# Kernel tuning notes

Measured on AMD Instinct MI355X. Metric: run time of the kernel, lower is better.

## Reference

```python
import jax, jax.numpy as jnp
import numpy as np
from jax import lax


def _kaiming_uniform(key, shape):
    fan_in = shape[1]
    bound = np.sqrt(6.0 / fan_in)
    return jax.random.uniform(key, shape, jnp.float32, -bound, bound)


def rbf_conv(x, w, k, pad):
    # x: [B,C,H,W]; w: [O, C*k*k]. Equivalent to F.unfold + torch.cdist (p=2).
    patches = lax.conv_general_dilated_patches(
        x, (k, k), (1, 1), [(pad, pad), (pad, pad)])  # [B, C*k*k, Ho, Wo]
    B, D, Ho, Wo = patches.shape
    p = patches.reshape(B, D, Ho * Wo)                 # [B, D, L]
    pn = jnp.sum(p * p, axis=1)                        # [B, L]
    wn = jnp.sum(w * w, axis=1)                        # [O]
    cross = jnp.einsum('bdl,od->bol', p, w)            # [B, O, L]
    d2 = pn[:, None, :] + wn[None, :, None] - 2.0 * cross
    d = jnp.sqrt(jnp.maximum(d2, 0.0))
    return d.reshape(B, w.shape[0], Ho, Wo)


def sfm(x, alpha):
    # non-overlapping (fh,fw) blocks, elementwise alpha weight, mean-pool
    B, C, H, W = x.shape
    fh, fw = alpha.shape
    xb = x.reshape(B, C, H // fh, fh, W // fw, fw).transpose(0, 1, 2, 4, 3, 5)
    return jnp.mean(xb * alpha, axis=(-2, -1))         # [B,C,H//fh,W//fw]


def gauss_act(d, std):
    return jnp.exp(d * d / (-2.0 * std * std))


def crelu(x, bias):
    return x * (x >= bias).astype(x.dtype)


def basic_block(x, w, std, bias, alpha, k, pad):
    d = rbf_conv(x, w, k, pad)
    return sfm(crelu(gauss_act(d, std), bias), alpha)


def setup_inputs() -> dict:
    key = jax.random.key(0)
    ks = jax.random.split(key, 8)
    x = jax.random.normal(ks[0], (16, 3, 128, 128), jnp.float32)
    w1 = _kaiming_uniform(ks[1], (96, 3 * 5 * 5))
    w2 = _kaiming_uniform(ks[2], (192, 96 * 5 * 5))
    w3 = _kaiming_uniform(ks[3], (384, 192 * 3 * 3))
    alpha = jnp.linspace(0.9, 0.99, 4, dtype=jnp.float32).reshape(2, 2)
    fc_w = jax.random.normal(ks[4], (100, 384 * 32 * 32), jnp.float32) * 0.01
    fc_b = jnp.zeros((100,), jnp.float32)
    return {
        'x': x,
        'w1': w1, 'std1': jnp.array([2.0], jnp.float32), 'bias1': jnp.array([0.3], jnp.float32), 'alpha1': alpha,
        'w2': w2, 'std2': jnp.array([2.0], jnp.float32), 'bias2': jnp.array([0.3], jnp.float32), 'alpha2': alpha,
        'w3': w3, 'std3': jnp.array([2.0], jnp.float32), 'bias3': jnp.array([0.3], jnp.float32),
        'fc_w': fc_w, 'fc_b': fc_b,
    }


def reference(x, w1, std1, bias1, alpha1, w2, std2, bias2, alpha2,
              w3, std3, bias3, fc_w, fc_b):
    h = basic_block(x, w1, std1, bias1, alpha1, 5, 2)      # [16,96,64,64]
    h = basic_block(h, w2, std2, bias2, alpha2, 5, 2)      # [16,192,32,32]
    d = rbf_conv(h, w3, 3, 1)                              # [16,384,32,32]
    h = crelu(gauss_act(d, std3), bias3)
    out = h.reshape(x.shape[0], -1) @ fc_w.T + fc_b        # [16,100]
    return out
```

## Files before the change

### kernel.cpp

```cpp
#include <hip/hip_runtime.h>

#define TPB 256

typedef short bf16x8 __attribute__((ext_vector_type(8)));
typedef float f32x4 __attribute__((ext_vector_type(4)));

__device__ inline unsigned short f2bf(float f) {
    unsigned int u = __float_as_uint(f);
    unsigned int r = (u + 0x7fffu + ((u >> 16) & 1u)) >> 16;
    return (unsigned short)r;
}
__device__ inline float bf2f(unsigned short h) {
    return __uint_as_float(((unsigned int)h) << 16);
}

__device__ __forceinline__ void gl16(void* lds, const void* g) {
    __builtin_amdgcn_global_load_lds(
        (const __attribute__((address_space(1))) unsigned int*)g,
        (__attribute__((address_space(3))) unsigned int*)lds, 16, 0, 0);
}

__global__ void prep_all(const float* __restrict__ x,
                         const float* __restrict__ w1, const float* __restrict__ w2,
                         const float* __restrict__ w3,
                         unsigned short* __restrict__ xbf,
                         unsigned short* __restrict__ w1r, unsigned short* __restrict__ w2r,
                         unsigned short* __restrict__ w3r, unsigned short* __restrict__ zerob,
                         float* __restrict__ wn1, float* __restrict__ wn2,
                         float* __restrict__ wn3) {
    int bid = blockIdx.x;
    int tid = threadIdx.x;
    if (bid < 1024) {
        int idx = bid * TPB + tid;
        int b = idx >> 14, px = idx & 16383;
        const float* xb = x + (size_t)b * 3 * 16384 + px;
        float v0 = xb[0], v1 = xb[16384], v2 = xb[32768];
        ushort4 v;
        v.x = f2bf(v0); v.y = f2bf(v1); v.z = f2bf(v2);
        v.w = f2bf(v0 * v0 + v1 * v1 + v2 * v2);
        *(ushort4*)&xbf[(size_t)idx * 4] = v;
    } else if (bid < 4388) {
        int idx = (bid - 1024) * TPB + tid;
        if (idx < 13056) {
            int o = idx / 136, d = idx - o * 136;
            int tp = d >> 2, c = d & 3;
            float v = 0.f;
            if (tp < 30) {
                int ki = tp / 6, kj = tp - 6 * ki;
                if (kj < 5) v = (c < 3) ? w1[o * 75 + c * 25 + ki * 5 + kj] : -0.5f;
            }
            w1r[idx] = f2bf(v);
        } else if (idx < 492288) {
            int i = idx - 13056;
            int c = i & 31; int r = i >> 5;
            int o = r % 192; r /= 192;
            int tap = r % 26; int cg = r / 26;
            float v = 0.f;
            if (tap < 25) v = w2[((size_t)o * 96 + cg * 32 + c) * 25 + tap];
            w2r[i] = f2bf(v);
        } else if (idx < 860928) {
            int i = idx - 492288;
            int c = i & 31; int r = i >> 5;
            int o = r % 192; r /= 192;
            int tap = r % 10; int cg = r / 10;
            float v = 0.f;
            if (tap < 9) v = w3[((size_t)o * 192 + cg * 32 + c) * 9 + tap];
            w3r[i] = f2bf(v);
        } else if (idx < 860992) {
            zerob[idx - 860928] = 0;
        }
    } else {
        int o = (bid - 4388) * 4 + (tid >> 6);
        int lane = tid & 63;
        const float* row; float* dst; int D;
        if (o < 96)       { row = w1 + (size_t)o * 75;           D = 75;   dst = wn1 + o; }
        else if (o < 288) { int r = o - 96;  row = w2 + (size_t)r * 2400; D = 2400; dst = wn2 + r; }
        else              { int r = o - 288; row = w3 + (size_t)r * 1728; D = 1728; dst = wn3 + r; }
        float acc = 0.f;
        for (int i = lane; i < D; i += 64) { float v = row[i]; acc += v * v; }
        #pragma unroll
        for (int off = 32; off >= 1; off >>= 1) acc += __shfl_down(acc, off);
        if (lane == 0) *dst = acc;
    }
}

__launch_bounds__(256, 2)
__global__ void conv1_mfma(const unsigned short* __restrict__ xbf,
                           const unsigned short* __restrict__ w1r,
                           const float* __restrict__ wn,
                           const float* __restrict__ stdp, const float* __restrict__ biasp,
                           const float* __restrict__ alphap,
                           unsigned short* __restrict__ out,
                           float* __restrict__ sqout)
{
    __shared__ unsigned short in_s[22 * 20 * 4];
    __shared__ unsigned short w_s[96 * 136];

    int bid = blockIdx.x;
    int tx = bid & 7; bid >>= 3;
    int ty = bid & 7; bid >>= 3;
    int b = bid;
    int x0 = tx * 16, y0 = ty * 16;
    int tid = threadIdx.x;
    int lane = tid & 63, wv = tid >> 6;
    int col = lane & 15, kg = lane >> 4;

    for (int idx = tid; idx < 21 * 20; idx += 256) {
        int py = idx / 20, px = idx - py * 20;
        int gy = y0 - 2 + py, gx = x0 - 2 + px;
        ushort4 v = make_ushort4(0, 0, 0, 0);
        if (gy >= 0 && gy < 128 && gx >= 0 && gx < 128)
            v = *(const ushort4*)&xbf[(((size_t)b * 128 + gy) * 128 + gx) * 4];
        *(ushort4*)&in_s[idx * 4] = v;
    }
    for (int idx = tid; idx < 1632; idx += 256)
        *(bf16x8*)&w_s[idx * 8] = *(const bf16x8*)&w1r[idx * 8];
    __syncthreads();

    f32x4 acc[6][4];
    #pragma unroll
    for (int mt = 0; mt < 6; ++mt)
        #pragma unroll
        for (int n = 0; n < 4; ++n) acc[mt][n] = (f32x4){0.f, 0.f, 0.f, 0.f};

    #pragma unroll
    for (int ks = 0; ks < 4; ++ks) {
        int tap0 = ks * 8 + kg * 2;
        int ki = tap0 / 6, kj = tap0 - 6 * ki;
        bf16x8 bfrag[4];
        #pragma unroll
        for (int n = 0; n < 4; ++n) {
            int row = wv * 4 + n + ki;
            int ix = col + kj;
            const unsigned short* p = &in_s[(row * 20 + ix) * 4];
            union { bf16x8 v; uint2 u[2]; } tmp;
            tmp.u[0] = *(const uint2*)p;
            tmp.u[1] = *(const uint2*)(p + 4);
            bfrag[n] = tmp.v;
        }
        bf16x8 afrag[6];
        #pragma unroll
        for (int mt = 0; mt < 6; ++mt)
            afrag[mt] = *(const bf16x8*)&w_s[(mt * 16 + col) * 136 + ks * 32 + kg * 8];
        #pragma unroll
        for (int mt = 0; mt < 6; ++mt)
            #pragma unroll
            for (int n = 0; n < 4; ++n)
                acc[mt][n] = __builtin_amdgcn_mfma_f32_16x16x32_bf16(
                    afrag[mt], bfrag[n], acc[mt][n], 0, 0, 0);
    }

    float stdv = stdp[0], biasv = biasp[0];
    float inv2s2 = 1.f / (2.f * stdv * stdv);
    float a00 = alphap[0], a01 = alphap[1], a10 = alphap[2], a11 = alphap[3];
    int dx = col & 1;
    float ax0 = dx ? a01 : a00;
    float ax1 = dx ? a11 : a10;

    float sqa[2] = {0.f, 0.f};
    #pragma unroll
    for (int mt = 0; mt < 6; ++mt) {
        #pragma unroll
        for (int p2 = 0; p2 < 2; ++p2) {
            unsigned short res[4];
            #pragma unroll
            for (int r = 0; r < 4; ++r) {
                int o = mt * 16 + kg * 4 + r;
                float wno = wn[o];
                float d20 = fmaxf(wno - 2.f * acc[mt][2 * p2][r], 0.f);
                float d21 = fmaxf(wno - 2.f * acc[mt][2 * p2 + 1][r], 0.f);
                float g0 = __expf(-d20 * inv2s2);
                float g1 = __expf(-d21 * inv2s2);
                g0 = (g0 >= biasv) ? g0 : 0.f;
                g1 = (g1 >= biasv) ? g1 : 0.f;
                float s = ax0 * g0 + ax1 * g1;
                s += __shfl_xor(s, 1);
                res[r] = f2bf(0.25f * s);
                float vv = bf2f(res[r]);
                sqa[p2] += vv * vv;
            }
            if (dx == 0) {
                int yo = ty * 8 + wv * 2 + p2, xo = tx * 8 + (col >> 1);
                *(ushort4*)&out[(((size_t)b * 64 + yo) * 64 + xo) * 96 + mt * 16 + kg * 4] =
                    make_ushort4(res[0], res[1], res[2], res[3]);
            }
        }
    }
    #pragma unroll
    for (int p2 = 0; p2 < 2; ++p2) {
        float s = sqa[p2];
        s += __shfl_xor(s, 16);
        s += __shfl_xor(s, 32);
        if (dx == 0 && kg == 0) {
            int yo = ty * 8 + wv * 2 + p2, xo = tx * 8 + (col >> 1);
            sqout[((size_t)b * 64 + yo) * 64 + xo] = s;
        }
    }
}

__launch_bounds__(128, 2)
__global__ void conv2_mfma(const unsigned short* __restrict__ hin,
                           const unsigned short* __restrict__ wt2,
                           const float* __restrict__ sq1,
                           const float* __restrict__ wn,
                           const float* __restrict__ stdp, const float* __restrict__ biasp,
                           const float* __restrict__ alphap,
                           const unsigned short* __restrict__ zerob,
                           unsigned short* __restrict__ hout)
{
    __shared__ unsigned short in_s[240 * 32];
    __shared__ unsigned short w_s[2][2 * 96 * 32];
    __shared__ float sq_s[12 * 20];
    __shared__ int s_nz[2];

    int bid = blockIdx.x;
    int xt = bid & 3; bid >>= 2;
    int yt = bid & 7; bid >>= 3;
    int ot = bid & 1; int b = bid >> 1;
    int x0 = xt * 16, y0 = yt * 8, o0 = ot * 96;
    int tid = threadIdx.x;
    int lane = tid & 63, wave_n = tid >> 6;
    int col = lane & 15, kg = lane >> 4;

    #pragma unroll
    for (int i = 0; i < 2; ++i) {
        int sidx = tid + i * 128;
        if (sidx < 240) {
            int r = sidx / 20, c = sidx - r * 20;
            int gy = y0 - 2 + r, gx = x0 - 2 + c;
            float v = 0.f;
            if (gy >= 0 && gy < 64 && gx >= 0 && gx < 64)
                v = sq1[((size_t)b * 64 + gy) * 64 + gx];
            sq_s[sidx] = v;
        }
    }

    f32x4 acc[6][4];
    #pragma unroll
    for (int mt = 0; mt < 6; ++mt)
        #pragma unroll
        for (int nt = 0; nt < 4; ++nt) acc[mt][nt] = (f32x4){0.f, 0.f, 0.f, 0.f};

    for (int cg = 0; cg < 3; ++cg) {
        #pragma unroll
        for (int i = 0; i < 8; ++i) {
            int chunk = tid + i * 128;
            if (chunk < 960) {
                int px = chunk >> 2, c16 = chunk & 3;
                int iy = px / 20, ix = px - iy * 20;
                int gy = y0 - 2 + iy, gx = x0 - 2 + ix;
                const void* src = (gy >= 0 && gy < 64 && gx >= 0 && gx < 64)
                    ? (const void*)&hin[(((size_t)b * 64 + gy) * 64 + gx) * 96 + cg * 32 + c16 * 8]
                    : (const void*)zerob;
                gl16(&in_s[chunk * 8], src);
            }
        }
        __syncthreads();

        unsigned int nzb = 0;
        #pragma unroll
        for (int i = 0; i < 8; ++i) {
            int chunk = tid + i * 128;
            if (chunk < 960) {
                uint4 v = *(const uint4*)&in_s[chunk * 8];
                nzb |= v.x | v.y | v.z | v.w;
            }
        }
        bool any = __any(nzb != 0);
        if (lane == 0) s_nz[wave_n] = any ? 1 : 0;
        __syncthreads();
        if (s_nz[0] | s_nz[1]) {
            #pragma unroll
            for (int i = 0; i < 6; ++i) {
                int chunk = tid + i * 128;
                int tp = chunk / 384, rem = chunk - tp * 384;
                gl16(&w_s[0][tp * 3072 + rem * 8],
                     &wt2[(((size_t)cg * 26 + tp) * 192 + o0) * 32 + rem * 8]);
            }
            __syncthreads();
            for (int pr = 0; pr < 13; ++pr) {
                int cur = pr & 1;
                if (pr < 12) {
                    #pragma unroll
                    for (int i = 0; i < 6; ++i) {
                        int chunk = tid + i * 128;
                        int tp = chunk / 384, rem = chunk - tp * 384;
                        gl16(&w_s[cur ^ 1][tp * 3072 + rem * 8],
                             &wt2[(((size_t)cg * 26 + (pr + 1) * 2 + tp) * 192 + o0) * 32 + rem * 8]);
                    }
                }
                #pragma unroll
                for (int t2 = 0; t2 < 2; ++t2) {
                    int tap = pr * 2 + t2;
                    int ki = tap / 5, kj = tap - 5 * ki;
                    if (tap >= 25) { ki = 0; kj = 0; }
                    bf16x8 bfrag[4], afrag[6];
                    #pragma unroll
                    for (int nt = 0; nt < 4; ++nt) {
                        int yy = 2 * nt + (col >> 3) + ki;
                        int xx = wave_n * 8 + (col & 7) + kj;
                        bfrag[nt] = *(const bf16x8*)&in_s[(yy * 20 + xx) * 32 + kg * 8];
                    }
                    #pragma unroll
                    for (int mt = 0; mt < 6; ++mt)
                        afrag[mt] = *(const bf16x8*)
                            &w_s[cur][(t2 * 96 + mt * 16 + col) * 32 + kg * 8];
                    #pragma unroll
                    for (int mt = 0; mt < 6; ++mt)
                        #pragma unroll
                        for (int nt = 0; nt < 4; ++nt)
                            acc[mt][nt] = __builtin_amdgcn_mfma_f32_16x16x32_bf16(
                                afrag[mt], bfrag[nt], acc[mt][nt], 0, 0, 0);
                }
                __syncthreads();
            }
        }
    }

    float stdv = stdp[0], biasv = biasp[0];
    float inv2s2 = 1.f / (2.f * stdv * stdv);
    float a_own = alphap[(col >> 3) * 2 + (col & 1)];
    #pragma unroll
    for (int nt = 0; nt < 4; ++nt) {
        int ly = 2 * nt + (col >> 3) + 2;
        int lx = wave_n * 8 + (col & 7) + 2;
        float pnv = 0.f;
        #pragma unroll
        for (int dy = -2; dy <= 2; ++dy)
            #pragma unroll
            for (int dx2 = -2; dx2 <= 2; ++dx2)
                pnv += sq_s[(ly + dy) * 20 + (lx + dx2)];
        int x = x0 + wave_n * 8 + (col & 7);
        int yo = (y0 >> 1) + nt;
        int xo = x >> 1;
        #pragma unroll
        for (int mt = 0; mt < 6; ++mt) {
            int ob = o0 + mt * 16 + (kg << 2);
            unsigned short res[4];
            #pragma unroll
            for (int r = 0; r < 4; ++r) {
                float d2 = fmaxf(pnv + wn[ob + r] - 2.f * acc[mt][nt][r], 0.f);
                float g = __expf(-d2 * inv2s2);
                g = (g >= biasv) ? g : 0.f;
                g *= a_own;
                g += __shfl_xor(g, 1);
                g += __shfl_xor(g, 8);
                res[r] = f2bf(0.25f * g);
            }
            if (((col & 1) == 0) && ((col & 8) == 0)) {
                *(ushort4*)&hout[(((size_t)b * 32 + yo) * 32 + xo) * 192 + ob] =
                    make_ushort4(res[0], res[1], res[2], res[3]);
            }
        }
    }
}

__launch_bounds__(256, 2)
__global__ void conv3_mfma(const unsigned short* __restrict__ hin,
                           const unsigned short* __restrict__ wt3,
                           const float* __restrict__ wn,
                           const float* __restrict__ stdp, const float* __restrict__ biasp,
                           const unsigned short* __restrict__ zerob,
                           unsigned short* __restrict__ hout)
{
    __shared__ unsigned short in_s[180 * 32];
    __shared__ unsigned short w_s[2][2 * 96 * 32];
    __shared__ float pnacc[180];

    int bid = blockIdx.x;
    int sp = bid & 7; bid >>= 3;
    int ot = bid & 3; int b = bid >> 2;
    int x0 = (sp & 1) * 16, y0 = (sp >> 1) * 8, o0 = ot * 96;
    int tid = threadIdx.x;
    int lane = tid & 63, wid = tid >> 6;
    int om = wid >> 1, wn2 = wid & 1;
    int col = lane & 15, kg = lane >> 4;
    int coly = col >> 3, colx = col & 7;

    if (tid < 180) pnacc[tid] = 0.f;

    f32x4 acc[3][4];
    #pragma unroll
    for (int mt = 0; mt < 3; ++mt)
        #pragma unroll
        for (int nt = 0; nt < 4; ++nt) acc[mt][nt] = (f32x4){0.f, 0.f, 0.f, 0.f};

    for (int cg = 0; cg < 6; ++cg) {
        #pragma unroll
        for (int i = 0; i < 3; ++i) {
            int chunk = tid + i * 256;
            if (chunk < 720) {
                int px = chunk >> 2, c16 = chunk & 3;
                int iy = px / 18, ix = px - iy * 18;
                int gy = y0 - 1 + iy, gx = x0 - 1 + ix;
                const void* src = (gy >= 0 && gy < 32 && gx >= 0 && gx < 32)
                    ? (const void*)&hin[(((size_t)b * 32 + gy) * 32 + gx) * 192 + cg * 32 + c16 * 8]
                    : (const void*)zerob;
                gl16(&in_s[chunk * 8], src);
            }
        }
        #pragma unroll
        for (int i = 0; i < 3; ++i) {
            int chunk = tid + i * 256;
            int tp = chunk / 384, rem = chunk - tp * 384;
            gl16(&w_s[0][tp * 3072 + rem * 8],
                 &wt3[(((size_t)cg * 10 + tp) * 192 + o0) * 32 + rem * 8]);
        }
        __syncthreads();

        if (tid < 180) {
            const unsigned short* p = &in_s[tid * 32];
            float a = 0.f;
            #pragma unroll
            for (int c = 0; c < 32; c += 8) {
                bf16x8 v = *(const bf16x8*)&p[c];
                #pragma unroll
                for (int j = 0; j < 8; ++j) { float f = bf2f((unsigned short)v[j]); a += f * f; }
            }
            pnacc[tid] += a;
        }

        for (int pr = 0; pr < 5; ++pr) {
            int cur = pr & 1;
            if (pr < 4) {
                #pragma unroll
                for (int i = 0; i < 3; ++i) {
                    int chunk = tid + i * 256;
                    int tp = chunk / 384, rem = chunk - tp * 384;
                    gl16(&w_s[cur ^ 1][tp * 3072 + rem * 8],
                         &wt3[(((size_t)cg * 10 + (pr + 1) * 2 + tp) * 192 + o0) * 32 + rem * 8]);
                }
            }
            #pragma unroll
            for (int t2 = 0; t2 < 2; ++t2) {
                int tap = pr * 2 + t2;
                int ki = tap / 3, kj = tap - 3 * ki;
                if (tap >= 9) { ki = 0; kj = 0; }
                bf16x8 bfrag[4], afrag[3];
                #pragma unroll
                for (int nt = 0; nt < 4; ++nt) {
                    int yy = 2 * nt + coly + ki;
                    int xx = wn2 * 8 + colx + kj;
                    bfrag[nt] = *(const bf16x8*)&in_s[(yy * 18 + xx) * 32 + kg * 8];
                }
                #pragma unroll
                for (int mt = 0; mt < 3; ++mt)
                    afrag[mt] = *(const bf16x8*)
                        &w_s[cur][(t2 * 96 + om * 48 + mt * 16 + col) * 32 + kg * 8];
                #pragma unroll
                for (int mt = 0; mt < 3; ++mt)
                    #pragma unroll
                    for (int nt = 0; nt < 4; ++nt)
                        acc[mt][nt] = __builtin_amdgcn_mfma_f32_16x16x32_bf16(
                            afrag[mt], bfrag[nt], acc[mt][nt], 0, 0, 0);
            }
            __syncthreads();
        }
    }

    float stdv = stdp[0], biasv = biasp[0];
    float inv2s2 = 1.f / (2.f * stdv * stdv);
    #pragma unroll
    for (int nt = 0; nt < 4; ++nt) {
        int y = y0 + 2 * nt + coly;
        int x = x0 + wn2 * 8 + colx;
        int ly = 2 * nt + coly + 1, lx = wn2 * 8 + colx + 1;
        float pnv = 0.f;
        #pragma unroll
        for (int dy = -1; dy <= 1; ++dy)
            #pragma unroll
            for (int dx = -1; dx <= 1; ++dx)
                pnv += pnacc[(ly + dy) * 18 + (lx + dx)];
        #pragma unroll
        for (int mt = 0; mt < 3; ++mt) {
            int ob = o0 + om * 48 + mt * 16 + (kg << 2);
            #pragma unroll
            for (int r = 0; r < 4; ++r) {
                float d2 = fmaxf(pnv + wn[ob + r] - 2.f * acc[mt][nt][r], 0.f);
                float g = __expf(-d2 * inv2s2);
                g = (g >= biasv) ? g : 0.f;
                hout[((size_t)b * 384 + ob + r) * 1024 + y * 32 + x] = f2bf(g);
            }
        }
    }
}

__launch_bounds__(256, 4)
__global__ void fc_mfma(const unsigned short* __restrict__ h3bf,
                        const float* __restrict__ fw,
                        float* __restrict__ fcp,
                        int* __restrict__ flags)
{
    __shared__ unsigned short h3s[16 * 520];
    __shared__ unsigned short fws[16 * 520];
    __shared__ float red[4][16][16];
    __shared__ int s_nz[4];
    const size_t KI = 393216;
    int ch = blockIdx.x;
    int i0 = ch * 512;
    int tid = threadIdx.x;
    int lane = tid & 63, wv = tid >> 6;
    int col = lane & 15, kg = lane >> 4;

    unsigned int nzbits = 0;
    #pragma unroll
    for (int it = 0; it < 4; ++it) {
        int c = tid + it * 256;
        int b = c >> 6, off = (c & 63) * 8;
        bf16x8 v = *(const bf16x8*)&h3bf[(size_t)b * KI + i0 + off];
        union { bf16x8 s; unsigned int u[4]; } cv; cv.s = v;
        nzbits |= cv.u[0] | cv.u[1] | cv.u[2] | cv.u[3];
        *(bf16x8*)&h3s[b * 520 + off] = v;
    }
    bool any = __any(nzbits != 0);
    if (lane == 0) s_nz[wv] = any ? 1 : 0;
    __syncthreads();
    int anyall = s_nz[0] | s_nz[1] | s_nz[2] | s_nz[3];
    if (!anyall) {
        if (tid == 0) flags[ch] = 0;
        return;
    }
    if (tid == 0) flags[ch] = 1;

    float4 pre[8];
    #pragma unroll
    for (int it = 0; it < 8; ++it) {
        int c = tid + it * 256;
        int row = c >> 7, off4 = (c & 127) * 4;
        pre[it] = (row < 100) ? *(const float4*)&fw[(size_t)row * KI + i0 + off4]
                              : make_float4(0.f, 0.f, 0.f, 0.f);
    }

    for (int jt = 0; jt < 7; ++jt) {
        int j0 = jt * 16;
        #pragma unroll
        for (int it = 0; it < 8; ++it) {
            int c = tid + it * 256;
            int row = c >> 7, off4 = (c & 127) * 4;
            *(ushort4*)&fws[row * 520 + off4] =
                make_ushort4(f2bf(pre[it].x), f2bf(pre[it].y), f2bf(pre[it].z), f2bf(pre[it].w));
        }
        if (jt < 6) {
            #pragma unroll
            for (int it = 0; it < 8; ++it) {
                int c = tid + it * 256;
                int row = c >> 7, off4 = (c & 127) * 4;
                int j = j0 + 16 + row;
                pre[it] = (j < 100) ? *(const float4*)&fw[(size_t)j * KI + i0 + off4]
                                    : make_float4(0.f, 0.f, 0.f, 0.f);
            }
        }
        __syncthreads();
        f32x4 acc = (f32x4){0.f, 0.f, 0.f, 0.f};
        #pragma unroll
        for (int s = 0; s < 4; ++s) {
            int k = wv * 128 + s * 32 + kg * 8;
            bf16x8 af = *(const bf16x8*)&fws[col * 520 + k];
            bf16x8 bg = *(const bf16x8*)&h3s[col * 520 + k];
            acc = __builtin_amdgcn_mfma_f32_16x16x32_bf16(af, bg, acc, 0, 0, 0);
        }
        #pragma unroll
        for (int r = 0; r < 4; ++r) red[wv][kg * 4 + r][col] = acc[r];
        __syncthreads();
        int j = tid >> 4, bb = tid & 15;
        float s = red[0][j][bb] + red[1][j][bb] + red[2][j][bb] + red[3][j][bb];
        fcp[((size_t)ch * 112 + j0 + j) * 16 + bb] = s;
    }
}

__global__ void fc_final(const float* __restrict__ fcp, const int* __restrict__ flags,
                         const float* __restrict__ fb, float* __restrict__ outp) {
    int j = blockIdx.x;
    int lane = threadIdx.x;
    float acc[16];
    #pragma unroll
    for (int b = 0; b < 16; ++b) acc[b] = 0.f;
    for (int ch = lane; ch < 768; ch += 64) {
        if (flags[ch]) {
            const float* p = &fcp[((size_t)ch * 112 + j) * 16];
            #pragma unroll
            for (int b = 0; b < 16; ++b) acc[b] += p[b];
        }
    }
    #pragma unroll
    for (int off = 32; off >= 1; off >>= 1)
        #pragma unroll
        for (int b = 0; b < 16; ++b) acc[b] += __shfl_down(acc[b], off);
    if (lane == 0) {
        float bj = fb[j];
        #pragma unroll
        for (int b = 0; b < 16; ++b) outp[b * 100 + j] = bj + acc[b];
    }
}

extern "C" void kernel_launch(void* const* d_in, const int* in_sizes, int n_in,
                              void* d_out, int out_size, void* d_ws, size_t ws_size,
                              hipStream_t stream) {
    const float* x      = (const float*)d_in[0];
    const float* w1     = (const float*)d_in[1];
    const float* std1   = (const float*)d_in[2];
    const float* bias1  = (const float*)d_in[3];
    const float* alpha1 = (const float*)d_in[4];
    const float* w2     = (const float*)d_in[5];
    const float* std2   = (const float*)d_in[6];
    const float* bias2  = (const float*)d_in[7];
    const float* alpha2 = (const float*)d_in[8];
    const float* w3     = (const float*)d_in[9];
    const float* std3   = (const float*)d_in[10];
    const float* bias3  = (const float*)d_in[11];
    const float* fc_w   = (const float*)d_in[12];
    const float* fc_b   = (const float*)d_in[13];
    float* out = (float*)d_out;
    float* ws  = (float*)d_ws;

    float* sbuf  = ws;
    float* fcp   = sbuf + 65536;
    float* wn1   = fcp + 1376256;
    float* wn2   = wn1 + 96;
    float* wn3   = wn2 + 192;
    int*   flags = (int*)(wn3 + 384);
    float* rest  = wn3 + 384 + 768 + 32;
    unsigned short* h1bf = (unsigned short*)rest;
    unsigned short* h2bf = h1bf + 6291456;
    unsigned short* h3bf = h2bf + 3145728;
    unsigned short* xbf  = h3bf + 6291456;
    unsigned short* w1r  = xbf + 1048576;
    unsigned short* w2r  = w1r + 13056;
    unsigned short* w3r  = w2r + 479232;
    unsigned short* zerob = w3r + 368640;

    dim3 B(TPB);

    prep_all<<<dim3(4556), B, 0, stream>>>(x, w1, w2, w3, xbf, w1r, w2r, w3r, zerob,
                                           wn1, wn2, wn3);

    conv1_mfma<<<dim3(1024), B, 0, stream>>>(xbf, w1r, wn1, std1, bias1, alpha1,
                                             h1bf, sbuf);

    conv2_mfma<<<dim3(1024), dim3(128), 0, stream>>>(
        h1bf, w2r, sbuf, wn2, std2, bias2, alpha2, zerob, h2bf);

    conv3_mfma<<<dim3(512), B, 0, stream>>>(
        h2bf, w3r, wn3, std3, bias3, zerob, h3bf);

    fc_mfma<<<dim3(768), B, 0, stream>>>(h3bf, fc_w, fcp, flags);
    fc_final<<<dim3(100), dim3(64), 0, stream>>>(fcp, flags, fc_b, out);
}
```

Measured before the change: 102.4 us.

## Fuse prep into conv1 and widen conv2 blocks to cover all output channels

The separate prep kernel is folded into conv1. Extra blocks now do the w2/w3 reorder and norm work, and conv1 blocks convert x and w1 to bf16 and compute the w1 norms in place, which drops one launch and the xbf/w1r round trip through memory. Conv2 now runs 256 threads per block covering all 192 output channels, so each input tile is loaded once instead of twice, at the cost of doubled weight LDS and half as many blocks. Each conv1 block repeats the w1 reorder and norm work, and the fused grid mixes unrelated work in one launch.

```diff
diff --git a/kernel.cpp b/kernel.cpp
--- a/kernel.cpp
+++ b/kernel.cpp
@@ -20,88 +20,64 @@
         (__attribute__((address_space(3))) unsigned int*)lds, 16, 0, 0);
 }
 
-__global__ void prep_all(const float* __restrict__ x,
-                         const float* __restrict__ w1, const float* __restrict__ w2,
-                         const float* __restrict__ w3,
-                         unsigned short* __restrict__ xbf,
-                         unsigned short* __restrict__ w1r, unsigned short* __restrict__ w2r,
-                         unsigned short* __restrict__ w3r, unsigned short* __restrict__ zerob,
-                         float* __restrict__ wn1, float* __restrict__ wn2,
-                         float* __restrict__ wn3) {
-    int bid = blockIdx.x;
-    int tid = threadIdx.x;
-    if (bid < 1024) {
-        int idx = bid * TPB + tid;
-        int b = idx >> 14, px = idx & 16383;
-        const float* xb = x + (size_t)b * 3 * 16384 + px;
-        float v0 = xb[0], v1 = xb[16384], v2 = xb[32768];
-        ushort4 v;
-        v.x = f2bf(v0); v.y = f2bf(v1); v.z = f2bf(v2);
-        v.w = f2bf(v0 * v0 + v1 * v1 + v2 * v2);
-        *(ushort4*)&xbf[(size_t)idx * 4] = v;
-    } else if (bid < 4388) {
-        int idx = (bid - 1024) * TPB + tid;
-        if (idx < 13056) {
-            int o = idx / 136, d = idx - o * 136;
-            int tp = d >> 2, c = d & 3;
-            float v = 0.f;
-            if (tp < 30) {
-                int ki = tp / 6, kj = tp - 6 * ki;
-                if (kj < 5) v = (c < 3) ? w1[o * 75 + c * 25 + ki * 5 + kj] : -0.5f;
-            }
-            w1r[idx] = f2bf(v);
-        } else if (idx < 492288) {
-            int i = idx - 13056;
-            int c = i & 31; int r = i >> 5;
-            int o = r % 192; r /= 192;
-            int tap = r % 26; int cg = r / 26;
-            float v = 0.f;
-            if (tap < 25) v = w2[((size_t)o * 96 + cg * 32 + c) * 25 + tap];
-            w2r[i] = f2bf(v);
-        } else if (idx < 860928) {
-            int i = idx - 492288;
-            int c = i & 31; int r = i >> 5;
-            int o = r % 192; r /= 192;
-            int tap = r % 10; int cg = r / 10;
-            float v = 0.f;
-            if (tap < 9) v = w3[((size_t)o * 192 + cg * 32 + c) * 9 + tap];
-            w3r[i] = f2bf(v);
-        } else if (idx < 860992) {
-            zerob[idx - 860928] = 0;
-        }
-    } else {
-        int o = (bid - 4388) * 4 + (tid >> 6);
-        int lane = tid & 63;
-        const float* row; float* dst; int D;
-        if (o < 96)       { row = w1 + (size_t)o * 75;           D = 75;   dst = wn1 + o; }
-        else if (o < 288) { int r = o - 96;  row = w2 + (size_t)r * 2400; D = 2400; dst = wn2 + r; }
-        else              { int r = o - 288; row = w3 + (size_t)r * 1728; D = 1728; dst = wn3 + r; }
-        float acc = 0.f;
-        for (int i = lane; i < D; i += 64) { float v = row[i]; acc += v * v; }
-        #pragma unroll
-        for (int off = 32; off >= 1; off >>= 1) acc += __shfl_down(acc, off);
-        if (lane == 0) *dst = acc;
-    }
-}
-
 __launch_bounds__(256, 2)
-__global__ void conv1_mfma(const unsigned short* __restrict__ xbf,
-                           const unsigned short* __restrict__ w1r,
-                           const float* __restrict__ wn,
+__global__ void conv1_prep(const float* __restrict__ x, const float* __restrict__ w1,
+                           const float* __restrict__ w2, const float* __restrict__ w3,
                            const float* __restrict__ stdp, const float* __restrict__ biasp,
                            const float* __restrict__ alphap,
+                           unsigned short* __restrict__ w2r, unsigned short* __restrict__ w3r,
+                           unsigned short* __restrict__ zerob,
+                           float* __restrict__ wn2, float* __restrict__ wn3,
                            unsigned short* __restrict__ out,
                            float* __restrict__ sqout)
 {
     __shared__ unsigned short in_s[22 * 20 * 4];
     __shared__ unsigned short w_s[96 * 136];
+    __shared__ float s_wn[96];
 
     int bid = blockIdx.x;
+    int tid = threadIdx.x;
+
+    if (bid >= 1024) {
+        if (bid < 4337) {
+            int idx = (bid - 1024) * TPB + tid;
+            if (idx < 479232) {
+                int c = idx & 31; int r = idx >> 5;
+                int o = r % 192; r /= 192;
+                int tap = r % 26; int cg = r / 26;
+                float v = 0.f;
+                if (tap < 25) v = w2[((size_t)o * 96 + cg * 32 + c) * 25 + tap];
+                w2r[idx] = f2bf(v);
+            } else if (idx < 847872) {
+                int i = idx - 479232;
+                int c = i & 31; int r = i >> 5;
+                int o = r % 192; r /= 192;
+                int tap = r % 10; int cg = r / 10;
+                float v = 0.f;
+                if (tap < 9) v = w3[((size_t)o * 192 + cg * 32 + c) * 9 + tap];
+                w3r[i] = f2bf(v);
+            } else if (idx < 847936) {
+                zerob[idx - 847872] = 0;
+            }
+        } else {
+            int o = 96 + (bid - 4337) * 4 + (tid >> 6);
+            int lane = tid & 63;
+            const float* row; float* dst; int D;
+            if (o < 288) { int r = o - 96;  row = w2 + (size_t)r * 2400; D = 2400; dst = wn2 + r; }
+            else         { int r = o - 288; row = w3 + (size_t)r * 1728; D = 1728; dst = wn3 + r; }
+            float acc = 0.f;
+            for (int i = lane; i < D; i += 64) { float v = row[i]; acc += v * v; }
+            #pragma unroll
+            for (int off = 32; off >= 1; off >>= 1) acc += __shfl_down(acc, off);
+            if (lane == 0) *dst = acc;
+        }
+        return;
+    }
+
     int tx = bid & 7; bid >>= 3;
     int ty = bid & 7; bid >>= 3;
     int b = bid;
     int x0 = tx * 16, y0 = ty * 16;
-    int tid = threadIdx.x;
     int lane = tid & 63, wv = tid >> 6;
     int col = lane & 15, kg = lane >> 4;
 
@@ -109,12 +85,31 @@
         int py = idx / 20, px = idx - py * 20;
         int gy = y0 - 2 + py, gx = x0 - 2 + px;
         ushort4 v = make_ushort4(0, 0, 0, 0);
-        if (gy >= 0 && gy < 128 && gx >= 0 && gx < 128)
-            v = *(const ushort4*)&xbf[(((size_t)b * 128 + gy) * 128 + gx) * 4];
+        if (gy >= 0 && gy < 128 && gx >= 0 && gx < 128) {
+            const float* xb = x + (size_t)b * 3 * 16384 + gy * 128 + gx;
+            float v0 = xb[0], v1 = xb[16384], v2 = xb[32768];
+            v = make_ushort4(f2bf(v0), f2bf(v1), f2bf(v2), f2bf(v0 * v0 + v1 * v1 + v2 * v2));
+        }
         *(ushort4*)&in_s[idx * 4] = v;
     }
-    for (int idx = tid; idx < 1632; idx += 256)
-        *(bf16x8*)&w_s[idx * 8] = *(const bf16x8*)&w1r[idx * 8];
+    for (int idx = tid; idx < 13056; idx += 256) {
+        int o = idx / 136, d = idx - o * 136;
+        int tp = d >> 2, c = d & 3;
+        float v = 0.f;
+        if (tp < 30) {
+            int ki = tp / 6, kj = tp - 6 * ki;
+            if (kj < 5) v = (c < 3) ? w1[o * 75 + c * 25 + ki * 5 + kj] : -0.5f;
+        }
+        w_s[idx] = f2bf(v);
+    }
+    if (tid < 192) {
+        int row = tid >> 1, half = tid & 1;
+        int i0 = half ? 38 : 0, i1 = half ? 75 : 38;
+        float a = 0.f;
+        for (int i = i0; i < i1; ++i) { float v = w1[row * 75 + i]; a += v * v; }
+        a += __shfl_xor(a, 1);
+        if (half == 0) s_wn[row] = a;
+    }
     __syncthreads();
 
     f32x4 acc[6][4];
@@ -166,7 +161,7 @@
             #pragma unroll
             for (int r = 0; r < 4; ++r) {
                 int o = mt * 16 + kg * 4 + r;
-                float wno = wn[o];
+                float wno = s_wn[o];
                 float d20 = fmaxf(wno - 2.f * acc[mt][2 * p2][r], 0.f);
                 float d21 = fmaxf(wno - 2.f * acc[mt][2 * p2 + 1][r], 0.f);
                 float g0 = __expf(-d20 * inv2s2);
@@ -198,7 +193,7 @@
     }
 }
 
-__launch_bounds__(128, 2)
+__launch_bounds__(256, 2)
 __global__ void conv2_mfma(const unsigned short* __restrict__ hin,
                            const unsigned short* __restrict__ wt2,
                            const float* __restrict__ sq1,
@@ -209,30 +204,28 @@
                            unsigned short* __restrict__ hout)
 {
     __shared__ unsigned short in_s[240 * 32];
-    __shared__ unsigned short w_s[2][2 * 96 * 32];
-    __shared__ float sq_s[12 * 20];
-    __shared__ int s_nz[2];
+    __shared__ unsigned short w_s[2][2 * 192 * 32];
+    __shared__ float sq_s[240];
+    __shared__ int s_nz[4];
 
     int bid = blockIdx.x;
     int xt = bid & 3; bid >>= 2;
     int yt = bid & 7; bid >>= 3;
-    int ot = bid & 1; int b = bid >> 1;
-    int x0 = xt * 16, y0 = yt * 8, o0 = ot * 96;
+    int b = bid;
+    int x0 = xt * 16, y0 = yt * 8;
     int tid = threadIdx.x;
-    int lane = tid & 63, wave_n = tid >> 6;
+    int lane = tid & 63, wid = tid >> 6;
+    int wave_m = wid >> 1, wave_n = wid & 1;
     int col = lane & 15, kg = lane >> 4;
-
-    #pragma unroll
-    for (int i = 0; i < 2; ++i) {
-        int sidx = tid + i * 128;
-        if (sidx < 240) {
-            int r = sidx / 20, c = sidx - r * 20;
-            int gy = y0 - 2 + r, gx = x0 - 2 + c;
-            float v = 0.f;
-            if (gy >= 0 && gy < 64 && gx >= 0 && gx < 64)
-                v = sq1[((size_t)b * 64 + gy) * 64 + gx];
-            sq_s[sidx] = v;
-        }
+    int coly = col >> 3, colx = col & 7;
+
+    if (tid < 240) {
+        int r = tid / 20, c = tid - r * 20;
+        int gy = y0 - 2 + r, gx = x0 - 2 + c;
+        float v = 0.f;
+        if (gy >= 0 && gy < 64 && gx >= 0 && gx < 64)
+            v = sq1[((size_t)b * 64 + gy) * 64 + gx];
+        sq_s[tid] = v;
     }
 
     f32x4 acc[6][4];
@@ -243,8 +236,8 @@
 
     for (int cg = 0; cg < 3; ++cg) {
         #pragma unroll
-        for (int i = 0; i < 8; ++i) {
-            int chunk = tid + i * 128;
+        for (int i = 0; i < 4; ++i) {
+            int chunk = tid + i * 256;
             if (chunk < 960) {
                 int px = chunk >> 2, c16 = chunk & 3;
                 int iy = px / 20, ix = px - iy * 20;
@@ -259,23 +252,23 @@
 
         unsigned int nzb = 0;
         #pragma unroll
-        for (int i = 0; i < 8; ++i) {
-            int chunk = tid + i * 128;
+        for (int i = 0; i < 4; ++i) {
+            int chunk = tid + i * 256;
             if (chunk < 960) {
                 uint4 v = *(const uint4*)&in_s[chunk * 8];
                 nzb |= v.x | v.y | v.z | v.w;
             }
         }
         bool any = __any(nzb != 0);
-        if (lane == 0) s_nz[wave_n] = any ? 1 : 0;
+        if (lane == 0) s_nz[wid] = any ? 1 : 0;
         __syncthreads();
-        if (s_nz[0] | s_nz[1]) {
+        if (s_nz[0] | s_nz[1] | s_nz[2] | s_nz[3]) {
             #pragma unroll
             for (int i = 0; i < 6; ++i) {
-                int chunk = tid + i * 128;
-                int tp = chunk / 384, rem = chunk - tp * 384;
-                gl16(&w_s[0][tp * 3072 + rem * 8],
-                     &wt2[(((size_t)cg * 26 + tp) * 192 + o0) * 32 + rem * 8]);
+                int chunk = tid + i * 256;
+                int tp = chunk / 768, rem = chunk - tp * 768;
+                gl16(&w_s[0][tp * 6144 + rem * 8],
+                     &wt2[(((size_t)cg * 26 + tp) * 192) * 32 + rem * 8]);
             }
             __syncthreads();
             for (int pr = 0; pr < 13; ++pr) {
@@ -283,10 +276,10 @@
                 if (pr < 12) {
                     #pragma unroll
                     for (int i = 0; i < 6; ++i) {
-                        int chunk = tid + i * 128;
-                        int tp = chunk / 384, rem = chunk - tp * 384;
-                        gl16(&w_s[cur ^ 1][tp * 3072 + rem * 8],
-                             &wt2[(((size_t)cg * 26 + (pr + 1) * 2 + tp) * 192 + o0) * 32 + rem * 8]);
+                        int chunk = tid + i * 256;
+                        int tp = chunk / 768, rem = chunk - tp * 768;
+                        gl16(&w_s[cur ^ 1][tp * 6144 + rem * 8],
+                             &wt2[(((size_t)cg * 26 + (pr + 1) * 2 + tp) * 192) * 32 + rem * 8]);
                     }
                 }
                 #pragma unroll
@@ -297,14 +290,14 @@
                     bf16x8 bfrag[4], afrag[6];
                     #pragma unroll
                     for (int nt = 0; nt < 4; ++nt) {
-                        int yy = 2 * nt + (col >> 3) + ki;
-                        int xx = wave_n * 8 + (col & 7) + kj;
+                        int yy = 2 * nt + coly + ki;
+                        int xx = wave_n * 8 + colx + kj;
                         bfrag[nt] = *(const bf16x8*)&in_s[(yy * 20 + xx) * 32 + kg * 8];
                     }
                     #pragma unroll
                     for (int mt = 0; mt < 6; ++mt)
                         afrag[mt] = *(const bf16x8*)
-                            &w_s[cur][(t2 * 96 + mt * 16 + col) * 32 + kg * 8];
+                            &w_s[cur][t2 * 6144 + (wave_m * 96 + mt * 16 + col) * 32 + kg * 8];
                     #pragma unroll
                     for (int mt = 0; mt < 6; ++mt)
                         #pragma unroll
@@ -319,23 +312,23 @@
 
     float stdv = stdp[0], biasv = biasp[0];
     float inv2s2 = 1.f / (2.f * stdv * stdv);
-    float a_own = alphap[(col >> 3) * 2 + (col & 1)];
+    float a_own = alphap[coly * 2 + (col & 1)];
     #pragma unroll
     for (int nt = 0; nt < 4; ++nt) {
-        int ly = 2 * nt + (col >> 3) + 2;
-        int lx = wave_n * 8 + (col & 7) + 2;
+        int ly = 2 * nt + coly + 2;
+        int lx = wave_n * 8 + colx + 2;
         float pnv = 0.f;
         #pragma unroll
         for (int dy = -2; dy <= 2; ++dy)
             #pragma unroll
             for (int dx2 = -2; dx2 <= 2; ++dx2)
                 pnv += sq_s[(ly + dy) * 20 + (lx + dx2)];
-        int x = x0 + wave_n * 8 + (col & 7);
+        int x = x0 + wave_n * 8 + colx;
         int yo = (y0 >> 1) + nt;
         int xo = x >> 1;
         #pragma unroll
         for (int mt = 0; mt < 6; ++mt) {
-            int ob = o0 + mt * 16 + (kg << 2);
+            int ob = wave_m * 96 + mt * 16 + (kg << 2);
             unsigned short res[4];
             #pragma unroll
             for (int r = 0; r < 4; ++r) {
@@ -615,29 +608,23 @@
 
     float* sbuf  = ws;
     float* fcp   = sbuf + 65536;
-    float* wn1   = fcp + 1376256;
-    float* wn2   = wn1 + 96;
+    float* wn2   = fcp + 1376256;
     float* wn3   = wn2 + 192;
     int*   flags = (int*)(wn3 + 384);
     float* rest  = wn3 + 384 + 768 + 32;
     unsigned short* h1bf = (unsigned short*)rest;
     unsigned short* h2bf = h1bf + 6291456;
     unsigned short* h3bf = h2bf + 3145728;
-    unsigned short* xbf  = h3bf + 6291456;
-    unsigned short* w1r  = xbf + 1048576;
-    unsigned short* w2r  = w1r + 13056;
+    unsigned short* w2r  = h3bf + 6291456;
     unsigned short* w3r  = w2r + 479232;
     unsigned short* zerob = w3r + 368640;
 
     dim3 B(TPB);
 
-    prep_all<<<dim3(4556), B, 0, stream>>>(x, w1, w2, w3, xbf, w1r, w2r, w3r, zerob,
-                                           wn1, wn2, wn3);
-
-    conv1_mfma<<<dim3(1024), B, 0, stream>>>(xbf, w1r, wn1, std1, bias1, alpha1,
-                                             h1bf, sbuf);
-
-    conv2_mfma<<<dim3(1024), dim3(128), 0, stream>>>(
+    conv1_prep<<<dim3(4481), B, 0, stream>>>(x, w1, w2, w3, std1, bias1, alpha1,
+                                             w2r, w3r, zerob, wn2, wn3, h1bf, sbuf);
+
+    conv2_mfma<<<dim3(512), B, 0, stream>>>(
         h1bf, w2r, sbuf, wn2, std2, bias2, alpha2, zerob, h2bf);
 
     conv3_mfma<<<dim3(512), B, 0, stream>>>(
```

Result: slower. 129.0 us (+26.0%).

## Cover all 192 output channels per conv2 block with four waves

Applied to the files above, without the earlier changes.

Each conv2 block now uses 256 threads in a 2x2 wave grid that together compute all 192 output channels, where before two blocks each handled 96 channels. The input tile and squared-norm halo are loaded once per spatial tile instead of twice, which halves input LDS fills and global reads. The cost is a doubled weight LDS buffer (about 48KB for weights plus the input tile), fewer blocks (512), and possibly lower occupancy.

```diff
diff --git a/kernel.cpp b/kernel.cpp
--- a/kernel.cpp
+++ b/kernel.cpp
@@ -198,7 +198,7 @@
     }
 }
 
-__launch_bounds__(128, 2)
+__launch_bounds__(256, 2)
 __global__ void conv2_mfma(const unsigned short* __restrict__ hin,
                            const unsigned short* __restrict__ wt2,
                            const float* __restrict__ sq1,
@@ -209,30 +209,28 @@
                            unsigned short* __restrict__ hout)
 {
     __shared__ unsigned short in_s[240 * 32];
-    __shared__ unsigned short w_s[2][2 * 96 * 32];
-    __shared__ float sq_s[12 * 20];
-    __shared__ int s_nz[2];
+    __shared__ unsigned short w_s[2][2 * 192 * 32];
+    __shared__ float sq_s[240];
+    __shared__ int s_nz[4];
 
     int bid = blockIdx.x;
     int xt = bid & 3; bid >>= 2;
     int yt = bid & 7; bid >>= 3;
-    int ot = bid & 1; int b = bid >> 1;
-    int x0 = xt * 16, y0 = yt * 8, o0 = ot * 96;
+    int b = bid;
+    int x0 = xt * 16, y0 = yt * 8;
     int tid = threadIdx.x;
-    int lane = tid & 63, wave_n = tid >> 6;
+    int lane = tid & 63, wid = tid >> 6;
+    int wave_m = wid >> 1, wave_n = wid & 1;
     int col = lane & 15, kg = lane >> 4;
-
-    #pragma unroll
-    for (int i = 0; i < 2; ++i) {
-        int sidx = tid + i * 128;
-        if (sidx < 240) {
-            int r = sidx / 20, c = sidx - r * 20;
-            int gy = y0 - 2 + r, gx = x0 - 2 + c;
-            float v = 0.f;
-            if (gy >= 0 && gy < 64 && gx >= 0 && gx < 64)
-                v = sq1[((size_t)b * 64 + gy) * 64 + gx];
-            sq_s[sidx] = v;
-        }
+    int coly = col >> 3, colx = col & 7;
+
+    if (tid < 240) {
+        int r = tid / 20, c = tid - r * 20;
+        int gy = y0 - 2 + r, gx = x0 - 2 + c;
+        float v = 0.f;
+        if (gy >= 0 && gy < 64 && gx >= 0 && gx < 64)
+            v = sq1[((size_t)b * 64 + gy) * 64 + gx];
+        sq_s[tid] = v;
     }
 
     f32x4 acc[6][4];
@@ -243,8 +241,8 @@
 
     for (int cg = 0; cg < 3; ++cg) {
         #pragma unroll
-        for (int i = 0; i < 8; ++i) {
-            int chunk = tid + i * 128;
+        for (int i = 0; i < 4; ++i) {
+            int chunk = tid + i * 256;
             if (chunk < 960) {
                 int px = chunk >> 2, c16 = chunk & 3;
                 int iy = px / 20, ix = px - iy * 20;
@@ -259,23 +257,23 @@
 
         unsigned int nzb = 0;
         #pragma unroll
-        for (int i = 0; i < 8; ++i) {
-            int chunk = tid + i * 128;
+        for (int i = 0; i < 4; ++i) {
+            int chunk = tid + i * 256;
             if (chunk < 960) {
                 uint4 v = *(const uint4*)&in_s[chunk * 8];
                 nzb |= v.x | v.y | v.z | v.w;
             }
         }
         bool any = __any(nzb != 0);
-        if (lane == 0) s_nz[wave_n] = any ? 1 : 0;
+        if (lane == 0) s_nz[wid] = any ? 1 : 0;
         __syncthreads();
-        if (s_nz[0] | s_nz[1]) {
+        if (s_nz[0] | s_nz[1] | s_nz[2] | s_nz[3]) {
             #pragma unroll
             for (int i = 0; i < 6; ++i) {
-                int chunk = tid + i * 128;
-                int tp = chunk / 384, rem = chunk - tp * 384;
-                gl16(&w_s[0][tp * 3072 + rem * 8],
-                     &wt2[(((size_t)cg * 26 + tp) * 192 + o0) * 32 + rem * 8]);
+                int chunk = tid + i * 256;
+                int tp = chunk / 768, rem = chunk - tp * 768;
+                gl16(&w_s[0][tp * 6144 + rem * 8],
+                     &wt2[(((size_t)cg * 26 + tp) * 192) * 32 + rem * 8]);
             }
             __syncthreads();
             for (int pr = 0; pr < 13; ++pr) {
@@ -283,10 +281,10 @@
                 if (pr < 12) {
                     #pragma unroll
                     for (int i = 0; i < 6; ++i) {
-                        int chunk = tid + i * 128;
-                        int tp = chunk / 384, rem = chunk - tp * 384;
-                        gl16(&w_s[cur ^ 1][tp * 3072 + rem * 8],
-                             &wt2[(((size_t)cg * 26 + (pr + 1) * 2 + tp) * 192 + o0) * 32 + rem * 8]);
+                        int chunk = tid + i * 256;
+                        int tp = chunk / 768, rem = chunk - tp * 768;
+                        gl16(&w_s[cur ^ 1][tp * 6144 + rem * 8],
+                             &wt2[(((size_t)cg * 26 + (pr + 1) * 2 + tp) * 192) * 32 + rem * 8]);
                     }
                 }
                 #pragma unroll
@@ -297,14 +295,14 @@
                     bf16x8 bfrag[4], afrag[6];
                     #pragma unroll
                     for (int nt = 0; nt < 4; ++nt) {
-                        int yy = 2 * nt + (col >> 3) + ki;
-                        int xx = wave_n * 8 + (col & 7) + kj;
+                        int yy = 2 * nt + coly + ki;
+                        int xx = wave_n * 8 + colx + kj;
                         bfrag[nt] = *(const bf16x8*)&in_s[(yy * 20 + xx) * 32 + kg * 8];
                     }
                     #pragma unroll
                     for (int mt = 0; mt < 6; ++mt)
                         afrag[mt] = *(const bf16x8*)
-                            &w_s[cur][(t2 * 96 + mt * 16 + col) * 32 + kg * 8];
+                            &w_s[cur][t2 * 6144 + (wave_m * 96 + mt * 16 + col) * 32 + kg * 8];
                     #pragma unroll
                     for (int mt = 0; mt < 6; ++mt)
                         #pragma unroll
@@ -319,23 +317,23 @@
 
     float stdv = stdp[0], biasv = biasp[0];
     float inv2s2 = 1.f / (2.f * stdv * stdv);
-    float a_own = alphap[(col >> 3) * 2 + (col & 1)];
+    float a_own = alphap[coly * 2 + (col & 1)];
     #pragma unroll
     for (int nt = 0; nt < 4; ++nt) {
-        int ly = 2 * nt + (col >> 3) + 2;
-        int lx = wave_n * 8 + (col & 7) + 2;
+        int ly = 2 * nt + coly + 2;
+        int lx = wave_n * 8 + colx + 2;
         float pnv = 0.f;
         #pragma unroll
         for (int dy = -2; dy <= 2; ++dy)
             #pragma unroll
             for (int dx2 = -2; dx2 <= 2; ++dx2)
                 pnv += sq_s[(ly + dy) * 20 + (lx + dx2)];
-        int x = x0 + wave_n * 8 + (col & 7);
+        int x = x0 + wave_n * 8 + colx;
         int yo = (y0 >> 1) + nt;
         int xo = x >> 1;
         #pragma unroll
         for (int mt = 0; mt < 6; ++mt) {
-            int ob = o0 + mt * 16 + (kg << 2);
+            int ob = wave_m * 96 + mt * 16 + (kg << 2);
             unsigned short res[4];
             #pragma unroll
             for (int r = 0; r < 4; ++r) {
@@ -637,7 +635,7 @@
     conv1_mfma<<<dim3(1024), B, 0, stream>>>(xbf, w1r, wn1, std1, bias1, alpha1,
                                              h1bf, sbuf);
 
-    conv2_mfma<<<dim3(1024), dim3(128), 0, stream>>>(
+    conv2_mfma<<<dim3(512), B, 0, stream>>>(
         h1bf, w2r, sbuf, wn2, std2, bias2, alpha2, zerob, h2bf);
 
     conv3_mfma<<<dim3(512), B, 0, stream>>>(
```

Measured after the change: 100.9 us (median of 2 runs). About the same (-1.4%).
